# Kernel tuning notes

Measured on AMD Instinct MI355X. Metric: run time of the kernel, lower is better.

Reference implementation:

```python
import jax, jax.numpy as jnp
import numpy as np

B, S, D, H, G, K = 4, 4096, 1024, 16, 4, 3
DG = D // G   # group channels = 256
DH = D // H   # head channels = 64


def setup_inputs() -> dict:
    key = jax.random.key(0)
    ks = jax.random.split(key, 8)
    def w(k, shape, std=0.02):
        return jax.random.normal(k, shape, jnp.float32) * std
    return {
        "x": jax.random.normal(ks[0], (B, S, D), jnp.float32),
        "Wq": w(ks[1], (D, D)), "bq": jnp.zeros((D,), jnp.float32),
        "Wk": w(ks[2], (D, D)), "bk": jnp.zeros((D,), jnp.float32),
        "Wv": w(ks[3], (D, D)), "bv": jnp.zeros((D,), jnp.float32),
        "Wo": w(ks[4], (D, D)), "bo": jnp.zeros((D,), jnp.float32),
        "Woff1": w(ks[5], (DG, DG, K)), "boff1": jnp.zeros((DG,), jnp.float32),
        "Woff2": w(ks[6], (DG,)),
        "bias_table": w(ks[7], (1, 1, S)),
    }


def reference(x, Wq, bq, Wk, bk, Wv, bv, Wo, bo, Woff1, boff1, Woff2, bias_table):
    bsz, seq, d = x.shape
    scale = d ** (-0.5)
    xc = jnp.transpose(x, (0, 2, 1))  # [B, D, S]

    # 1x1 conv projections == channel GEMMs
    q = jnp.einsum('oc,bcs->bos', Wq, xc) + bq[None, :, None]  # [B, D, S]

    # group: [B*G, DG, S]
    gq = q.reshape(bsz * G, DG, seq)
    # offset head: conv1d(k=3, pad=1) -> conv1d(k=1, no bias) -> [B*G, S]
    h = jax.lax.conv_general_dilated(
        gq, Woff1, window_strides=(1,), padding=((K // 2, K // 2),),
        dimension_numbers=('NCH', 'OIH', 'NCH')) + boff1[None, :, None]
    offset = jnp.einsum('c,bcs->bs', Woff2, h)
    offset = jnp.tanh(offset) * K  # offset_range_factor = kernel

    gx = xc.reshape(bsz * G, DG, seq)  # grouped x

    # faithful replication of _grid_sample_1d: F.grid_sample on feats [N,C,S,1]
    # with grid (x = vgrid_scaled -> width dim of size 1, y = 0 -> height dim of
    # size S), bilinear, zero padding, align_corners=False.
    grid = jnp.arange(seq, dtype=x.dtype)[None, :]
    vgrid_scaled = 2.0 * (grid + offset) / max(seq - 1, 1) - 1.0  # [B*G, S]
    ix = vgrid_scaled / 2.0                 # unnormalized width coord (W=1)
    wx = jnp.clip(1.0 - jnp.abs(ix), 0.0, 1.0)  # bilinear weight on width idx 0
    iy = (seq - 1) / 2.0                    # unnormalized height coord for y=0
    y0 = int(np.floor(iy)); y1 = min(y0 + 1, seq - 1)
    wy1 = float(iy - y0); wy0 = 1.0 - wy1
    feat_c = wy0 * gx[:, :, y0] + wy1 * gx[:, :, y1]  # [B*G, DG]
    x_sampled = feat_c[:, :, None] * wx[:, None, :]   # [B*G, DG, S]
    xs = x_sampled.reshape(bsz, d, seq)               # ungroup -> [B, D, S]

    k = jnp.einsum('oc,bcs->bos', Wk, xs) + bk[None, :, None]
    v = jnp.einsum('oc,bcs->bos', Wv, xs) + bv[None, :, None]

    qh = q.reshape(bsz * H, DH, seq)
    kh = k.reshape(bsz * H, DH, seq)
    vh = v.reshape(bsz * H, DH, seq) + bias_table[:, :, :seq]

    # channel attention: contract over sequence dim (as in the original einsum)
    scores = jnp.einsum('bis,bjs->bij', qh, kh) * scale  # [B*H, DH, DH]
    attn = jax.nn.softmax(scores, axis=-1)
    out = jnp.einsum('bij,bjs->bis', attn, vh)           # [B*H, DH, S]
    out = out.reshape(bsz, d, seq).transpose(0, 2, 1)     # [B, S, D]
    return jnp.einsum('bsd,od->bso', out, Wo) + bo
```

## Files before the change

### kernel.cpp

```cpp
#include <hip/hip_runtime.h>
#include <math.h>

#define BB 4
#define SS 4096
#define DD 1024
#define HH 16
#define GG 4
#define KK 3
#define DG 256
#define DH 64

enum : size_t {
  OFF_WEFF  = 0,
  OFF_OFFC  = 1024,
  OFF_WEQ   = 1280,
  OFF_ZT    = 13568,
  OFF_WX    = 210176,
  OFF_XWP   = 275712,
  OFF_XW    = 1586432,
  OFF_XS    = 1602816,
  OFF_SW    = 1606912,
  OFF_FEAT  = 1607168,
  OFF_KF    = 1611264,
  OFF_VF    = 1627648,
  OFF_QW    = 1644032,
  OFF_QS    = 1660416,
  OFF_AV    = 1664512,
  OFF_AB    = 1680896,
  OFF_C2    = 1684992,
  OFF_WAV   = 1689088,
  OFF_WOSUM = 1705472,
  WS_FLOATS = 1706496
};

__device__ __forceinline__ float wred_sum(float v) {
#pragma unroll
  for (int o = 32; o > 0; o >>= 1) v += __shfl_xor(v, o, 64);
  return v;
}
__device__ __forceinline__ float wred_max(float v) {
#pragma unroll
  for (int o = 32; o > 0; o >>= 1) v = fmaxf(v, __shfl_xor(v, o, 64));
  return v;
}

__global__ void k_pre1(const float* __restrict__ Woff1, const float* __restrict__ Woff2,
                       const float* __restrict__ x, const float* __restrict__ Wo,
                       float* __restrict__ ws) {
  const int t = threadIdx.x;
  const int lane = t & 63;
  if (blockIdx.x < 192) {
    const int widx = (blockIdx.x * 256 + t) >> 6;
    const int i = widx / 3, kk = widx - 3 * i;
    float a = 0.f;
#pragma unroll
    for (int u = 0; u < 4; ++u) {
      const int cc = lane + 64 * u;
      a += Woff2[cc] * Woff1[(size_t)(cc * DG + i) * KK + kk];
    }
    a = wred_sum(a);
    if (lane == 0) ws[OFF_WEFF + widx] = a;
  } else if (blockIdx.x < 208) {
    const int gid = (blockIdx.x - 192) * 256 + t;
    const int b = gid >> 10, c = gid & 1023;
    ws[OFF_FEAT + gid] = 0.5f * (x[((size_t)b * SS + 2047) * DD + c] +
                                 x[((size_t)b * SS + 2048) * DD + c]);
  } else {
    const int o = ((blockIdx.x - 208) * 256 + t) >> 6;
    const float4* wo = (const float4*)(Wo + (size_t)o * DD);
    float v = 0.f;
#pragma unroll
    for (int it = 0; it < 4; ++it) {
      const float4 a = wo[lane + 64 * it];
      v += a.x + a.y + a.z + a.w;
    }
    v = wred_sum(v);
    if (lane == 0) ws[OFF_WOSUM + o] = v;
  }
}

__global__ void k_pre2(const float* __restrict__ Wq, const float* __restrict__ bq,
                       const float* __restrict__ Woff2, const float* __restrict__ boff1,
                       float* __restrict__ ws) {
  const float* Weff = ws + OFF_WEFF;
  const int t = threadIdx.x;
  const int lane = t & 63;
  if (blockIdx.x < 192) {
    const int j = blockIdx.x >> 4;
    const int c0 = (blockIdx.x & 15) * 64;
    const int g = j / 3, kk = j - 3 * g;
    const int q = t >> 6;
    float a = 0.f;
#pragma unroll 4
    for (int ii = 0; ii < 64; ++ii) {
      const int i = q * 64 + ii;
      a += Weff[i * KK + kk] * Wq[(size_t)(g * DG + i) * DD + c0 + lane];
    }
    __shared__ float red[4][64];
    red[q][lane] = a;
    __syncthreads();
    if (q == 0) {
      const float v = red[0][lane] + red[1][lane] + red[2][lane] + red[3][lane];
      ws[OFF_WEQ + (size_t)j * DD + c0 + lane] = v;
    }
  } else {
    if (t >= 64) return;
    float beff = 0.f;
#pragma unroll
    for (int u = 0; u < 4; ++u) {
      const int cc = lane + 64 * u;
      beff += Woff2[cc] * boff1[cc];
    }
    beff = wred_sum(beff);
#pragma unroll
    for (int g = 0; g < 4; ++g) {
      float a = 0.f;
#pragma unroll
      for (int u = 0; u < 4; ++u) {
        const int i = lane + 64 * u;
        a += (Weff[i * 3 + 0] + Weff[i * 3 + 1] + Weff[i * 3 + 2]) * bq[g * DG + i];
      }
      a = wred_sum(a);
      if (lane == 0) ws[OFF_OFFC + g] = a + beff;
    }
  }
}

__global__ __launch_bounds__(256, 2) void k_z(const float* __restrict__ x,
                                              const float* __restrict__ weq,
                                              float* __restrict__ zt) {
  const int lane = threadIdx.x & 63;
  const int wave = (blockIdx.x * blockDim.x + threadIdx.x) >> 6;
  const int nwaves = (gridDim.x * blockDim.x) >> 6;
  float4 w[12][4];
#pragma unroll
  for (int j = 0; j < 12; ++j)
#pragma unroll
    for (int it = 0; it < 4; ++it)
      w[j][it] = *(const float4*)(weq + (size_t)j * DD + 4 * (lane + 64 * it));
  for (int row = wave; row < BB * SS; row += nwaves) {
    const float4* xr = (const float4*)(x + (size_t)row * DD);
    float4 xv[4];
#pragma unroll
    for (int it = 0; it < 4; ++it) xv[it] = xr[lane + 64 * it];
    float acc[12];
#pragma unroll
    for (int j = 0; j < 12; ++j) {
      float a = 0.f;
#pragma unroll
      for (int it = 0; it < 4; ++it)
        a += xv[it].x * w[j][it].x + xv[it].y * w[j][it].y +
             xv[it].z * w[j][it].z + xv[it].w * w[j][it].w;
      acc[j] = a;
    }
#pragma unroll
    for (int j = 0; j < 12; ++j) acc[j] = wred_sum(acc[j]);
    if (lane == 0) {
#pragma unroll
      for (int j = 0; j < 12; ++j) zt[(size_t)row * 12 + j] = acc[j];
    }
  }
}

__global__ void k_wx(float* __restrict__ ws) {
  const int gid = blockIdx.x * blockDim.x + threadIdx.x;
  if (gid >= BB * GG * SS) return;
  const int s = gid & (SS - 1);
  const int g = (gid >> 12) & 3;
  const int b = gid >> 14;
  const float* z = ws + OFF_ZT + (size_t)b * SS * 12;
  float off = ws[OFF_OFFC + g];
  if (s > 0)      off += z[(size_t)(s - 1) * 12 + g * 3 + 0];
  off += z[(size_t)s * 12 + g * 3 + 1];
  if (s < SS - 1) off += z[(size_t)(s + 1) * 12 + g * 3 + 2];
  off = tanhf(off) * (float)KK;
  const float vg = 2.0f * ((float)s + off) / (float)(SS - 1) - 1.0f;
  const float ix = 0.5f * vg;
  float wv = 1.0f - fabsf(ix);
  wv = fminf(fmaxf(wv, 0.0f), 1.0f);
  ws[OFF_WX + (size_t)(b * GG + g) * SS + s] = wv;
}

__global__ __launch_bounds__(256) void k_xw_part(const float* __restrict__ x,
                                                 float* __restrict__ ws) {
  const float* wx = ws + OFF_WX;
  const int b = blockIdx.x >> 6;
  const int ch = blockIdx.x & 63;
  const int t = threadIdx.x;
  float4 aw[5] = {};
  const int s0 = ch * 64;
#pragma unroll 4
  for (int si = 0; si < 64; ++si) {
    const int s = s0 + si;
    const float w0 = wx[(size_t)(b * GG + 0) * SS + s];
    const float w1 = wx[(size_t)(b * GG + 1) * SS + s];
    const float w2 = wx[(size_t)(b * GG + 2) * SS + s];
    const float w3 = wx[(size_t)(b * GG + 3) * SS + s];
    const float4 f = *(const float4*)(x + (size_t)(b * SS + s) * DD + 4 * t);
    aw[0].x += f.x * w0; aw[0].y += f.y * w0; aw[0].z += f.z * w0; aw[0].w += f.w * w0;
    aw[1].x += f.x * w1; aw[1].y += f.y * w1; aw[1].z += f.z * w1; aw[1].w += f.w * w1;
    aw[2].x += f.x * w2; aw[2].y += f.y * w2; aw[2].z += f.z * w2; aw[2].w += f.w * w2;
    aw[3].x += f.x * w3; aw[3].y += f.y * w3; aw[3].z += f.z * w3; aw[3].w += f.w * w3;
    aw[4].x += f.x; aw[4].y += f.y; aw[4].z += f.z; aw[4].w += f.w;
  }
  float* Xwp = ws + OFF_XWP;
#pragma unroll
  for (int slot = 0; slot < 5; ++slot)
    *(float4*)(Xwp + (((size_t)(b * 5 + slot) * 64 + ch) * DD) + 4 * t) = aw[slot];
}

__global__ void k_xw_red(float* __restrict__ ws) {
  const int t = threadIdx.x;
  const int lane = t & 63;
  if (blockIdx.x < 320) {
    const int b = blockIdx.x / 80;
    const int rem = blockIdx.x - b * 80;
    const int slot = rem >> 4;
    const int c0 = (rem & 15) * 64;
    const int q = t >> 6;
    const float* base = ws + OFF_XWP + (size_t)(b * 5 + slot) * 64 * DD;
    float a = 0.f;
#pragma unroll 4
    for (int ii = 0; ii < 16; ++ii) {
      const int ch = q * 16 + ii;
      a += base[(size_t)ch * DD + c0 + lane];
    }
    __shared__ float red[4][64];
    red[q][lane] = a;
    __syncthreads();
    if (q == 0) {
      const float v = red[0][lane] + red[1][lane] + red[2][lane] + red[3][lane];
      if (slot < 4) ws[OFF_XW + ((size_t)(b * GG + slot)) * DD + c0 + lane] = v;
      else          ws[OFF_XS + (size_t)b * DD + c0 + lane] = v;
    }
  } else {
    const int w = blockIdx.x - 320;
    const float* wx = ws + OFF_WX + (size_t)w * SS;
    float a = 0.f;
#pragma unroll 4
    for (int it = 0; it < 16; ++it) a += wx[t + 256 * it];
    a = wred_sum(a);
    __shared__ float red[4];
    if (lane == 0) red[t >> 6] = a;
    __syncthreads();
    if (t == 0) ws[OFF_SW + w] = red[0] + red[1] + red[2] + red[3];
  }
}

__global__ void k_dots(const float* __restrict__ Wq, const float* __restrict__ bq,
                       const float* __restrict__ Wk, const float* __restrict__ Wv,
                       float* __restrict__ ws) {
  const int lane = threadIdx.x & 63;
  const int w = (blockIdx.x * blockDim.x + threadIdx.x) >> 6;
  if (w < 16384) {
    const int o = w & 1023, g = (w >> 10) & 3, b = w >> 12;
    const float4 a = ((const float4*)(Wk + (size_t)o * DD + g * DG))[lane];
    const float4 f = ((const float4*)(ws + OFF_FEAT + b * DD + g * DG))[lane];
    float v = a.x * f.x + a.y * f.y + a.z * f.z + a.w * f.w;
    v = wred_sum(v);
    if (lane == 0) ws[OFF_KF + w] = v;
  } else if (w < 32768) {
    const int i2 = w - 16384;
    const int o = i2 & 1023, g = (i2 >> 10) & 3, b = i2 >> 12;
    const float4 a = ((const float4*)(Wv + (size_t)o * DD + g * DG))[lane];
    const float4 f = ((const float4*)(ws + OFF_FEAT + b * DD + g * DG))[lane];
    float v = a.x * f.x + a.y * f.y + a.z * f.z + a.w * f.w;
    v = wred_sum(v);
    if (lane == 0) ws[OFF_VF + i2] = v;
  } else if (w < 49152) {
    const int i2 = w - 32768;
    const int g = i2 & 3, I = (i2 >> 2) & 1023, b = i2 >> 12;
    const float4* wq = (const float4*)(Wq + (size_t)I * DD);
    const float4* xw = (const float4*)(ws + OFF_XW + (size_t)(b * GG + g) * DD);
    float v = 0.f;
#pragma unroll
    for (int it = 0; it < 4; ++it) {
      const float4 a = wq[lane + 64 * it], c = xw[lane + 64 * it];
      v += a.x * c.x + a.y * c.y + a.z * c.z + a.w * c.w;
    }
    v = wred_sum(v);
    if (lane == 0) ws[OFF_QW + i2] = v + bq[I] * ws[OFF_SW + b * GG + g];
  } else if (w < 53248) {
    const int i2 = w - 49152;
    const int I = i2 & 1023, b = i2 >> 10;
    const float4* wq = (const float4*)(Wq + (size_t)I * DD);
    const float4* xs = (const float4*)(ws + OFF_XS + (size_t)b * DD);
    float v = 0.f;
#pragma unroll
    for (int it = 0; it < 4; ++it) {
      const float4 a = wq[lane + 64 * it], c = xs[lane + 64 * it];
      v += a.x * c.x + a.y * c.y + a.z * c.z + a.w * c.w;
    }
    v = wred_sum(v);
    if (lane == 0) ws[OFF_QS + i2] = v + (float)SS * bq[I];
  }
}

__global__ void k_attn(const float* __restrict__ bk, const float* __restrict__ bv,
                       float* __restrict__ ws) {
  const int gid = blockIdx.x * blockDim.x + threadIdx.x;
  const int lane = gid & 63;
  const int w = gid >> 6;
  if (w >= BB * DD) return;
  const int b = w >> 10, d = w & 1023;
  const int hh = d >> 6;
  const int J = (hh << 6) | lane;
  const float* Qw = ws + OFF_QW + (size_t)w * 4;
  const float q0 = Qw[0], q1 = Qw[1], q2 = Qw[2], q3 = Qw[3];
  const float qs = ws[OFF_QS + w];
  const float* Kf = ws + OFF_KF + (size_t)b * GG * DD;
  float sc = q0 * Kf[0 * DD + J] + q1 * Kf[1 * DD + J] +
             q2 * Kf[2 * DD + J] + q3 * Kf[3 * DD + J] + bk[J] * qs;
  sc *= 0.03125f;
  const float m = wred_max(sc);
  const float e = expf(sc - m);
  const float sum = wred_sum(e);
  const float attn = e / sum;
  const float* Vf = ws + OFF_VF + (size_t)b * GG * DD;
#pragma unroll
  for (int g = 0; g < 4; ++g) {
    const float av = wred_sum(attn * Vf[(size_t)g * DD + J]);
    if (lane == 0) ws[OFF_AV + (size_t)w * 4 + g] = av;
  }
  const float ab = wred_sum(attn * bv[J]);
  if (lane == 0) ws[OFF_AB + w] = ab;
}

__global__ void k_wav(const float* __restrict__ Wo, const float* __restrict__ bo,
                      float* __restrict__ ws) {
  const int gid = blockIdx.x * blockDim.x + threadIdx.x;
  const int lane = gid & 63;
  const int w = gid >> 6;
  if (w >= BB * DD) return;
  const int b = w >> 10, o = w & 1023;
  float acc0 = 0, acc1 = 0, acc2 = 0, acc3 = 0, acc4 = 0;
  const float4* wo4 = (const float4*)(Wo + (size_t)o * DD);
  const float* AV = ws + OFF_AV + (size_t)b * DD * 4;
  const float* Ab = ws + OFF_AB + (size_t)b * DD;
#pragma unroll
  for (int it = 0; it < 4; ++it) {
    const int d4 = lane + 64 * it;
    const float4 wv = wo4[d4];
    const float4 a0 = *(const float4*)(AV + (size_t)(4 * d4 + 0) * 4);
    const float4 a1 = *(const float4*)(AV + (size_t)(4 * d4 + 1) * 4);
    const float4 a2 = *(const float4*)(AV + (size_t)(4 * d4 + 2) * 4);
    const float4 a3 = *(const float4*)(AV + (size_t)(4 * d4 + 3) * 4);
    acc0 += wv.x * a0.x + wv.y * a1.x + wv.z * a2.x + wv.w * a3.x;
    acc1 += wv.x * a0.y + wv.y * a1.y + wv.z * a2.y + wv.w * a3.y;
    acc2 += wv.x * a0.z + wv.y * a1.z + wv.z * a2.z + wv.w * a3.z;
    acc3 += wv.x * a0.w + wv.y * a1.w + wv.z * a2.w + wv.w * a3.w;
    const float4 abv = *(const float4*)(Ab + 4 * d4);
    acc4 += wv.x * abv.x + wv.y * abv.y + wv.z * abv.z + wv.w * abv.w;
  }
  acc0 = wred_sum(acc0); acc1 = wred_sum(acc1); acc2 = wred_sum(acc2);
  acc3 = wred_sum(acc3); acc4 = wred_sum(acc4);
  if (lane == 0) {
    float* WAV = ws + OFF_WAV + (size_t)w * 4;
    WAV[0] = acc0; WAV[1] = acc1; WAV[2] = acc2; WAV[3] = acc3;
    ws[OFF_C2 + w] = acc4 + bo[o];
  }
}

__global__ __launch_bounds__(256) void k_out(const float* __restrict__ btab,
                                             const float* __restrict__ ws,
                                             float* __restrict__ out) {
  const int b = blockIdx.x >> 7;
  const int ch = blockIdx.x & 127;
  const int t = threadIdx.x;
  const int o0 = 4 * t;
  float4 wav[4];
#pragma unroll
  for (int io = 0; io < 4; ++io)
    wav[io] = *(const float4*)(ws + OFF_WAV + (size_t)(b * DD + o0 + io) * 4);
  const float4 c24 = *(const float4*)(ws + OFF_C2 + (size_t)b * DD + o0);
  const float4 wos4 = *(const float4*)(ws + OFF_WOSUM + o0);
  const float* wx = ws + OFF_WX;
  const int s0 = ch * 32;
#pragma unroll 2
  for (int si = 0; si < 32; ++si) {
    const int s = s0 + si;
    const float w0 = wx[(size_t)(b * GG + 0) * SS + s];
    const float w1 = wx[(size_t)(b * GG + 1) * SS + s];
    const float w2 = wx[(size_t)(b * GG + 2) * SS + s];
    const float w3 = wx[(size_t)(b * GG + 3) * SS + s];
    const float bt = btab[s];
    float4 val;
    val.x = c24.x + bt * wos4.x + w0 * wav[0].x + w1 * wav[0].y + w2 * wav[0].z + w3 * wav[0].w;
    val.y = c24.y + bt * wos4.y + w0 * wav[1].x + w1 * wav[1].y + w2 * wav[1].z + w3 * wav[1].w;
    val.z = c24.z + bt * wos4.z + w0 * wav[2].x + w1 * wav[2].y + w2 * wav[2].z + w3 * wav[2].w;
    val.w = c24.w + bt * wos4.w + w0 * wav[3].x + w1 * wav[3].y + w2 * wav[3].z + w3 * wav[3].w;
    *(float4*)(out + (size_t)(b * SS + s) * DD + o0) = val;
  }
}

extern "C" void kernel_launch(void* const* d_in, const int* in_sizes, int n_in,
                              void* d_out, int out_size, void* d_ws, size_t ws_size,
                              hipStream_t stream) {
  const float* x     = (const float*)d_in[0];
  const float* Wq    = (const float*)d_in[1];
  const float* bq    = (const float*)d_in[2];
  const float* Wk    = (const float*)d_in[3];
  const float* bk    = (const float*)d_in[4];
  const float* Wv    = (const float*)d_in[5];
  const float* bv    = (const float*)d_in[6];
  const float* Wo    = (const float*)d_in[7];
  const float* bo    = (const float*)d_in[8];
  const float* Woff1 = (const float*)d_in[9];
  const float* boff1 = (const float*)d_in[10];
  const float* Woff2 = (const float*)d_in[11];
  const float* btab  = (const float*)d_in[12];
  float* ws  = (float*)d_ws;
  float* out = (float*)d_out;

  k_pre1<<<464, 256, 0, stream>>>(Woff1, Woff2, x, Wo, ws);
  k_pre2<<<193, 256, 0, stream>>>(Wq, bq, Woff2, boff1, ws);
  k_z<<<512, 256, 0, stream>>>(x, ws + OFF_WEQ, ws + OFF_ZT);
  k_wx<<<(BB * GG * SS) / 256, 256, 0, stream>>>(ws);
  k_xw_part<<<256, 256, 0, stream>>>(x, ws);
  k_xw_red<<<336, 256, 0, stream>>>(ws);
  k_dots<<<13312, 256, 0, stream>>>(Wq, bq, Wk, Wv, ws);
  k_attn<<<1024, 256, 0, stream>>>(bk, bv, ws);
  k_wav<<<1024, 256, 0, stream>>>(Wo, bo, ws);
  k_out<<<512, 256, 0, stream>>>(btab, ws, out);
}
```

Measured before the change: 217.3 us.

## Fuse offset projection, sampling weights and weighted x reduction into one kernel

Merges k_z, k_wx and k_xw_part into one chunked kernel. Each block computes the 12 projected values for its 32-row chunk plus halo rows into shared memory, derives the sampling weights locally, and accumulates the weighted x sums from the same rows. This removes two launches and the global round trip of the z and wx intermediates, and should let x rows be reused from cache. The cost is recomputing halo rows and a larger partial buffer for k_xw_red. k_dots is also restructured so each wave reuses a weight row across batches and groups, cutting the grid size, and k_out is split into twice as many smaller blocks.

```diff
diff --git a/kernel.cpp b/kernel.cpp
--- a/kernel.cpp
+++ b/kernel.cpp
@@ -9,28 +9,29 @@
 #define KK 3
 #define DG 256
 #define DH 64
+#define CH 32
+#define NCH (SS / CH)
 
 enum : size_t {
   OFF_WEFF  = 0,
   OFF_OFFC  = 1024,
   OFF_WEQ   = 1280,
-  OFF_ZT    = 13568,
-  OFF_WX    = 210176,
-  OFF_XWP   = 275712,
-  OFF_XW    = 1586432,
-  OFF_XS    = 1602816,
-  OFF_SW    = 1606912,
-  OFF_FEAT  = 1607168,
-  OFF_KF    = 1611264,
-  OFF_VF    = 1627648,
-  OFF_QW    = 1644032,
-  OFF_QS    = 1660416,
-  OFF_AV    = 1664512,
-  OFF_AB    = 1680896,
-  OFF_C2    = 1684992,
-  OFF_WAV   = 1689088,
-  OFF_WOSUM = 1705472,
-  WS_FLOATS = 1706496
+  OFF_WX    = 13568,
+  OFF_XWP   = 79104,
+  OFF_XW    = 2700544,
+  OFF_XS    = 2716928,
+  OFF_SW    = 2721024,
+  OFF_FEAT  = 2721280,
+  OFF_KF    = 2725376,
+  OFF_VF    = 2741760,
+  OFF_QW    = 2758144,
+  OFF_QS    = 2774528,
+  OFF_AV    = 2778624,
+  OFF_AB    = 2795008,
+  OFF_C2    = 2799104,
+  OFF_WAV   = 2803200,
+  OFF_WOSUM = 2819584,
+  WS_FLOATS = 2820608
 };
 
 __device__ __forceinline__ float wred_sum(float v) {
@@ -126,20 +127,29 @@
   }
 }
 
-__global__ __launch_bounds__(256, 2) void k_z(const float* __restrict__ x,
-                                              const float* __restrict__ weq,
-                                              float* __restrict__ zt) {
-  const int lane = threadIdx.x & 63;
-  const int wave = (blockIdx.x * blockDim.x + threadIdx.x) >> 6;
-  const int nwaves = (gridDim.x * blockDim.x) >> 6;
+__global__ __launch_bounds__(256, 2) void k_main(const float* __restrict__ x,
+                                                 float* __restrict__ ws) {
+  const int b = blockIdx.x >> 7;
+  const int chunk = blockIdx.x & 127;
+  const int s0 = chunk * CH;
+  const int t = threadIdx.x;
+  const int lane = t & 63;
+  const int wvid = t >> 6;
+  __shared__ float zsh[CH + 2][12];
+  __shared__ float wxs[4][CH];
+
+  const float* weq = ws + OFF_WEQ;
   float4 w[12][4];
 #pragma unroll
   for (int j = 0; j < 12; ++j)
 #pragma unroll
     for (int it = 0; it < 4; ++it)
       w[j][it] = *(const float4*)(weq + (size_t)j * DD + 4 * (lane + 64 * it));
-  for (int row = wave; row < BB * SS; row += nwaves) {
-    const float4* xr = (const float4*)(x + (size_t)row * DD);
+
+  for (int r = wvid; r < CH + 2; r += 4) {
+    const int s = s0 - 1 + r;
+    if (s < 0 || s >= SS) continue;
+    const float4* xr = (const float4*)(x + (size_t)(b * SS + s) * DD);
     float4 xv[4];
 #pragma unroll
     for (int it = 0; it < 4; ++it) xv[it] = xr[lane + 64 * it];
@@ -157,56 +167,44 @@
     for (int j = 0; j < 12; ++j) acc[j] = wred_sum(acc[j]);
     if (lane == 0) {
 #pragma unroll
-      for (int j = 0; j < 12; ++j) zt[(size_t)row * 12 + j] = acc[j];
-    }
-  }
-}
-
-__global__ void k_wx(float* __restrict__ ws) {
-  const int gid = blockIdx.x * blockDim.x + threadIdx.x;
-  if (gid >= BB * GG * SS) return;
-  const int s = gid & (SS - 1);
-  const int g = (gid >> 12) & 3;
-  const int b = gid >> 14;
-  const float* z = ws + OFF_ZT + (size_t)b * SS * 12;
-  float off = ws[OFF_OFFC + g];
-  if (s > 0)      off += z[(size_t)(s - 1) * 12 + g * 3 + 0];
-  off += z[(size_t)s * 12 + g * 3 + 1];
-  if (s < SS - 1) off += z[(size_t)(s + 1) * 12 + g * 3 + 2];
-  off = tanhf(off) * (float)KK;
-  const float vg = 2.0f * ((float)s + off) / (float)(SS - 1) - 1.0f;
-  const float ix = 0.5f * vg;
-  float wv = 1.0f - fabsf(ix);
-  wv = fminf(fmaxf(wv, 0.0f), 1.0f);
-  ws[OFF_WX + (size_t)(b * GG + g) * SS + s] = wv;
-}
-
-__global__ __launch_bounds__(256) void k_xw_part(const float* __restrict__ x,
-                                                 float* __restrict__ ws) {
-  const float* wx = ws + OFF_WX;
-  const int b = blockIdx.x >> 6;
-  const int ch = blockIdx.x & 63;
-  const int t = threadIdx.x;
+      for (int j = 0; j < 12; ++j) zsh[r][j] = acc[j];
+    }
+  }
+  __syncthreads();
+
+  if (t < CH) {
+    const int s = s0 + t;
+#pragma unroll
+    for (int g = 0; g < 4; ++g) {
+      float off = ws[OFF_OFFC + g];
+      if (s > 0)      off += zsh[t][g * 3 + 0];
+      off += zsh[t + 1][g * 3 + 1];
+      if (s < SS - 1) off += zsh[t + 2][g * 3 + 2];
+      off = tanhf(off) * (float)KK;
+      const float vg = 2.0f * ((float)s + off) / (float)(SS - 1) - 1.0f;
+      float wvv = 1.0f - fabsf(0.5f * vg);
+      wvv = fminf(fmaxf(wvv, 0.0f), 1.0f);
+      wxs[g][t] = wvv;
+      ws[OFF_WX + (size_t)(b * GG + g) * SS + s] = wvv;
+    }
+  }
+  __syncthreads();
+
   float4 aw[5] = {};
-  const int s0 = ch * 64;
 #pragma unroll 4
-  for (int si = 0; si < 64; ++si) {
+  for (int si = 0; si < CH; ++si) {
     const int s = s0 + si;
-    const float w0 = wx[(size_t)(b * GG + 0) * SS + s];
-    const float w1 = wx[(size_t)(b * GG + 1) * SS + s];
-    const float w2 = wx[(size_t)(b * GG + 2) * SS + s];
-    const float w3 = wx[(size_t)(b * GG + 3) * SS + s];
     const float4 f = *(const float4*)(x + (size_t)(b * SS + s) * DD + 4 * t);
+    const float w0 = wxs[0][si], w1 = wxs[1][si], w2 = wxs[2][si], w3 = wxs[3][si];
     aw[0].x += f.x * w0; aw[0].y += f.y * w0; aw[0].z += f.z * w0; aw[0].w += f.w * w0;
     aw[1].x += f.x * w1; aw[1].y += f.y * w1; aw[1].z += f.z * w1; aw[1].w += f.w * w1;
     aw[2].x += f.x * w2; aw[2].y += f.y * w2; aw[2].z += f.z * w2; aw[2].w += f.w * w2;
     aw[3].x += f.x * w3; aw[3].y += f.y * w3; aw[3].z += f.z * w3; aw[3].w += f.w * w3;
     aw[4].x += f.x; aw[4].y += f.y; aw[4].z += f.z; aw[4].w += f.w;
   }
-  float* Xwp = ws + OFF_XWP;
 #pragma unroll
   for (int slot = 0; slot < 5; ++slot)
-    *(float4*)(Xwp + (((size_t)(b * 5 + slot) * 64 + ch) * DD) + 4 * t) = aw[slot];
+    *(float4*)(ws + OFF_XWP + (((size_t)(b * 5 + slot) * NCH + chunk) * DD) + 4 * t) = aw[slot];
 }
 
 __global__ void k_xw_red(float* __restrict__ ws) {
@@ -218,11 +216,11 @@
     const int slot = rem >> 4;
     const int c0 = (rem & 15) * 64;
     const int q = t >> 6;
-    const float* base = ws + OFF_XWP + (size_t)(b * 5 + slot) * 64 * DD;
+    const float* base = ws + OFF_XWP + (size_t)(b * 5 + slot) * NCH * DD;
     float a = 0.f;
 #pragma unroll 4
-    for (int ii = 0; ii < 16; ++ii) {
-      const int ch = q * 16 + ii;
+    for (int ii = 0; ii < 32; ++ii) {
+      const int ch = q * 32 + ii;
       a += base[(size_t)ch * DD + c0 + lane];
     }
     __shared__ float red[4][64];
@@ -250,49 +248,61 @@
 __global__ void k_dots(const float* __restrict__ Wq, const float* __restrict__ bq,
                        const float* __restrict__ Wk, const float* __restrict__ Wv,
                        float* __restrict__ ws) {
-  const int lane = threadIdx.x & 63;
-  const int w = (blockIdx.x * blockDim.x + threadIdx.x) >> 6;
-  if (w < 16384) {
-    const int o = w & 1023, g = (w >> 10) & 3, b = w >> 12;
-    const float4 a = ((const float4*)(Wk + (size_t)o * DD + g * DG))[lane];
-    const float4 f = ((const float4*)(ws + OFF_FEAT + b * DD + g * DG))[lane];
-    float v = a.x * f.x + a.y * f.y + a.z * f.z + a.w * f.w;
-    v = wred_sum(v);
-    if (lane == 0) ws[OFF_KF + w] = v;
-  } else if (w < 32768) {
-    const int i2 = w - 16384;
-    const int o = i2 & 1023, g = (i2 >> 10) & 3, b = i2 >> 12;
-    const float4 a = ((const float4*)(Wv + (size_t)o * DD + g * DG))[lane];
-    const float4 f = ((const float4*)(ws + OFF_FEAT + b * DD + g * DG))[lane];
-    float v = a.x * f.x + a.y * f.y + a.z * f.z + a.w * f.w;
-    v = wred_sum(v);
-    if (lane == 0) ws[OFF_VF + i2] = v;
-  } else if (w < 49152) {
-    const int i2 = w - 32768;
-    const int g = i2 & 3, I = (i2 >> 2) & 1023, b = i2 >> 12;
+  const int t = threadIdx.x;
+  const int lane = t & 63;
+  if (blockIdx.x < 1024) {
+    const int widx = blockIdx.x * 4 + (t >> 6);
+    const int g = widx >> 10, o = widx & 1023;
+    const float4 ak = ((const float4*)(Wk + (size_t)o * DD + g * DG))[lane];
+    const float4 avv = ((const float4*)(Wv + (size_t)o * DD + g * DG))[lane];
+    float kk[4], vv[4];
+#pragma unroll
+    for (int b = 0; b < 4; ++b) {
+      const float4 f = ((const float4*)(ws + OFF_FEAT + (size_t)b * DD + g * DG))[lane];
+      kk[b] = ak.x * f.x + ak.y * f.y + ak.z * f.z + ak.w * f.w;
+      vv[b] = avv.x * f.x + avv.y * f.y + avv.z * f.z + avv.w * f.w;
+    }
+#pragma unroll
+    for (int b = 0; b < 4; ++b) { kk[b] = wred_sum(kk[b]); vv[b] = wred_sum(vv[b]); }
+    if (lane == 0) {
+#pragma unroll
+      for (int b = 0; b < 4; ++b) {
+        ws[OFF_KF + ((size_t)(b * GG + g)) * DD + o] = kk[b];
+        ws[OFF_VF + ((size_t)(b * GG + g)) * DD + o] = vv[b];
+      }
+    }
+  } else {
+    const int widx = (blockIdx.x - 1024) * 4 + (t >> 6);
+    const int b = widx >> 10, I = widx & 1023;
     const float4* wq = (const float4*)(Wq + (size_t)I * DD);
-    const float4* xw = (const float4*)(ws + OFF_XW + (size_t)(b * GG + g) * DD);
-    float v = 0.f;
+    float4 a[4];
+#pragma unroll
+    for (int it = 0; it < 4; ++it) a[it] = wq[lane + 64 * it];
+    float acc[5] = {0.f, 0.f, 0.f, 0.f, 0.f};
+#pragma unroll
+    for (int g = 0; g < 4; ++g) {
+      const float4* xw = (const float4*)(ws + OFF_XW + (size_t)(b * GG + g) * DD);
+#pragma unroll
+      for (int it = 0; it < 4; ++it) {
+        const float4 c = xw[lane + 64 * it];
+        acc[g] += a[it].x * c.x + a[it].y * c.y + a[it].z * c.z + a[it].w * c.w;
+      }
+    }
+    const float4* xs = (const float4*)(ws + OFF_XS + (size_t)b * DD);
 #pragma unroll
     for (int it = 0; it < 4; ++it) {
-      const float4 a = wq[lane + 64 * it], c = xw[lane + 64 * it];
-      v += a.x * c.x + a.y * c.y + a.z * c.z + a.w * c.w;
-    }
-    v = wred_sum(v);
-    if (lane == 0) ws[OFF_QW + i2] = v + bq[I] * ws[OFF_SW + b * GG + g];
-  } else if (w < 53248) {
-    const int i2 = w - 49152;
-    const int I = i2 & 1023, b = i2 >> 10;
-    const float4* wq = (const float4*)(Wq + (size_t)I * DD);
-    const float4* xs = (const float4*)(ws + OFF_XS + (size_t)b * DD);
-    float v = 0.f;
-#pragma unroll
-    for (int it = 0; it < 4; ++it) {
-      const float4 a = wq[lane + 64 * it], c = xs[lane + 64 * it];
-      v += a.x * c.x + a.y * c.y + a.z * c.z + a.w * c.w;
-    }
-    v = wred_sum(v);
-    if (lane == 0) ws[OFF_QS + i2] = v + (float)SS * bq[I];
+      const float4 c = xs[lane + 64 * it];
+      acc[4] += a[it].x * c.x + a[it].y * c.y + a[it].z * c.z + a[it].w * c.w;
+    }
+#pragma unroll
+    for (int u = 0; u < 5; ++u) acc[u] = wred_sum(acc[u]);
+    if (lane == 0) {
+      const float bqi = bq[I];
+#pragma unroll
+      for (int g = 0; g < 4; ++g)
+        ws[OFF_QW + ((size_t)(b * DD + I)) * 4 + g] = acc[g] + bqi * ws[OFF_SW + b * GG + g];
+      ws[OFF_QS + (size_t)b * DD + I] = acc[4] + (float)SS * bqi;
+    }
   }
 }
 
@@ -364,8 +374,8 @@
 __global__ __launch_bounds__(256) void k_out(const float* __restrict__ btab,
                                              const float* __restrict__ ws,
                                              float* __restrict__ out) {
-  const int b = blockIdx.x >> 7;
-  const int ch = blockIdx.x & 127;
+  const int b = blockIdx.x >> 8;
+  const int ch = blockIdx.x & 255;
   const int t = threadIdx.x;
   const int o0 = 4 * t;
   float4 wav[4];
@@ -375,9 +385,9 @@
   const float4 c24 = *(const float4*)(ws + OFF_C2 + (size_t)b * DD + o0);
   const float4 wos4 = *(const float4*)(ws + OFF_WOSUM + o0);
   const float* wx = ws + OFF_WX;
-  const int s0 = ch * 32;
+  const int s0 = ch * 16;
 #pragma unroll 2
-  for (int si = 0; si < 32; ++si) {
+  for (int si = 0; si < 16; ++si) {
     const int s = s0 + si;
     const float w0 = wx[(size_t)(b * GG + 0) * SS + s];
     const float w1 = wx[(size_t)(b * GG + 1) * SS + s];
@@ -414,12 +424,10 @@
 
   k_pre1<<<464, 256, 0, stream>>>(Woff1, Woff2, x, Wo, ws);
   k_pre2<<<193, 256, 0, stream>>>(Wq, bq, Woff2, boff1, ws);
-  k_z<<<512, 256, 0, stream>>>(x, ws + OFF_WEQ, ws + OFF_ZT);
-  k_wx<<<(BB * GG * SS) / 256, 256, 0, stream>>>(ws);
-  k_xw_part<<<256, 256, 0, stream>>>(x, ws);
+  k_main<<<512, 256, 0, stream>>>(x, ws);
   k_xw_red<<<336, 256, 0, stream>>>(ws);
-  k_dots<<<13312, 256, 0, stream>>>(Wq, bq, Wk, Wv, ws);
+  k_dots<<<2048, 256, 0, stream>>>(Wq, bq, Wk, Wv, ws);
   k_attn<<<1024, 256, 0, stream>>>(bk, bv, ws);
   k_wav<<<1024, 256, 0, stream>>>(Wo, bo, ws);
-  k_out<<<512, 256, 0, stream>>>(btab, ws, out);
-}
+  k_out<<<1024, 256, 0, stream>>>(btab, ws, out);
+}
```

Result: no change. 217.4 us (+0.0%).
